# Kernel optimization log

Measured on AMD Instinct MI355X. Metric: run time of the kernel, lower is better.

The kernel has to match this reference:

```python
import jax, jax.numpy as jnp
import numpy as np

NUM_USERS = 100000
NUM_ITEMS = 50000
N_NODES = NUM_USERS + NUM_ITEMS
N_EDGES = 2400000
EMB = 64
BATCH = 4096
GCN_LAYERS = 3
TAU = 0.2
SSL_LAMBDA = 0.1
REG_LAMBDA = 1e-4


def setup_inputs() -> dict:
    key = jax.random.key(0)
    ks = jax.random.split(key, 8)
    user = jax.random.randint(ks[0], (BATCH,), 0, NUM_USERS, dtype=jnp.int32)
    pos_item = jax.random.randint(ks[1], (BATCH,), 0, NUM_ITEMS, dtype=jnp.int32)
    neg_item = jax.random.randint(ks[2], (BATCH,), 0, NUM_ITEMS, dtype=jnp.int32)
    # symmetric bipartite edges: user -> item and item -> user
    half = N_EDGES // 2
    src_u = jax.random.randint(ks[3], (half,), 0, NUM_USERS, dtype=jnp.int32)
    dst_i = jax.random.randint(ks[4], (half,), NUM_USERS, N_NODES, dtype=jnp.int32)
    adj_row = jnp.concatenate([src_u, dst_i])
    adj_col = jnp.concatenate([dst_i, src_u])
    # normalized-adjacency-like small positive values
    adj_val = jax.random.uniform(ks[5], (N_EDGES,), dtype=jnp.float32) * 0.01
    user_emb_w = jax.random.normal(ks[6], (NUM_USERS, EMB), dtype=jnp.float32) * 0.1
    item_emb_w = jax.random.normal(ks[7], (NUM_ITEMS, EMB), dtype=jnp.float32) * 0.1
    return {"user": user, "pos_item": pos_item, "neg_item": neg_item,
            "adj_row": adj_row, "adj_col": adj_col, "adj_val": adj_val,
            "user_emb_w": user_emb_w, "item_emb_w": item_emb_w}


def _aggregate(adj_row, adj_col, adj_val, user_emb_w, item_emb_w):
    emb = jnp.concatenate([user_emb_w, item_emb_w], axis=0)  # [N, d]
    acc = emb
    e = emb
    for _ in range(GCN_LAYERS):
        # sparse.mm(adj, e): gather columns, scale, scatter-add into rows
        e = jax.ops.segment_sum(adj_val[:, None] * e[adj_col], adj_row,
                                num_segments=N_NODES)
        acc = acc + e
    final = acc / (GCN_LAYERS + 1)  # mean over stacked layer outputs
    return final[:NUM_USERS], final[NUM_USERS:]


def reference(user, pos_item, neg_item, adj_row, adj_col, adj_val,
              user_emb_w, item_emb_w):
    user_all, item_all = _aggregate(adj_row, adj_col, adj_val,
                                    user_emb_w, item_emb_w)
    u = user_all[user]          # [B, d]
    pos = item_all[pos_item]    # [B, d]
    neg = item_all[neg_item]    # [B, d]
    # BPR loss
    pos_s = jnp.sum(u * pos, axis=-1)
    neg_s = jnp.sum(u * neg, axis=-1)
    bpr_loss = -jnp.mean(jax.nn.log_sigmoid(pos_s - neg_s))
    # L2 regularization
    b = u.shape[0]
    reg_loss = 0.5 * (jnp.sum(u * u) + jnp.sum(pos * pos) + jnp.sum(neg * neg)) / b
    reg_loss = reg_loss * REG_LAMBDA
    # neighbor-aggregate SSL (InfoNCE between user and its positive item)
    un = u / jnp.linalg.norm(u, axis=-1, keepdims=True)
    pn = pos / jnp.linalg.norm(pos, axis=-1, keepdims=True)
    logits = un @ pn.T / TAU                       # [B, B]
    pos_logit = jnp.diagonal(logits)
    na_loss = jnp.mean(jax.nn.logsumexp(logits, axis=1) - pos_logit) * SSL_LAMBDA
    return bpr_loss + reg_loss + na_loss
```

## Files before the change

### kernel.cpp

```cpp
#include <hip/hip_runtime.h>
#include <hip/hip_fp16.h>
#include <math.h>

#define NUM_USERS 100000
#define NUM_ITEMS 50000
#define N_NODES   150000
#define N_EDGES   2400000
#define HALF_E    (N_EDGES / 2)
#define EMB       64
#define BATCH     4096
#define TAU        0.2f
#define SSL_LAMBDA 0.1f
#define REG_LAMBDA 1e-4f

#define NB        293
#define BROWS     512
#define CAP       13632
#define BINA_BLK  512

__device__ __forceinline__ float wave_sum(float v) {
    #pragma unroll
    for (int m = 1; m < 64; m <<= 1) v += __shfl_xor(v, m, 64);
    return v;
}
__device__ __forceinline__ __half2 bits2h2(int b) {
    union { int i; __half2 h; } u; u.i = b; return u.h;
}
__device__ __forceinline__ int h22bits(__half2 h) {
    union { int i; __half2 h; } u; u.h = h; return u.i;
}
__device__ __forceinline__ float h2f(unsigned short s) {
    union { unsigned short s; __half h; } u; u.s = s; return __half2float(u.h);
}

__global__ __launch_bounds__(256) void cast_h0(
        const float4* __restrict__ uw, const float4* __restrict__ iw,
        uint2* __restrict__ h) {
    size_t i = (size_t)blockIdx.x * 256 + threadIdx.x;
    const size_t tot = (size_t)N_NODES * EMB / 4;
    if (i >= tot) return;
    const size_t nu = (size_t)NUM_USERS * EMB / 4;
    float4 v = (i < nu) ? uw[i] : iw[i - nu];
    h[i] = make_uint2(h22bits(__floats2half2_rn(v.x, v.y)),
                      h22bits(__floats2half2_rn(v.z, v.w)));
}

__global__ __launch_bounds__(256) void bin_scatter(
        const int* __restrict__ row, const int* __restrict__ col,
        const float* __restrict__ val,
        int* __restrict__ bucket_cursor, int2* __restrict__ arena) {
    __shared__ int hist[NB];
    const int t = threadIdx.x;
    for (int i = t; i < NB; i += 256) hist[i] = 0;
    __syncthreads();
    const int per = (HALF_E + gridDim.x - 1) / gridDim.x;
    const int beg = blockIdx.x * per;
    const int end = min(beg + per, HALF_E);
    for (int e = beg + t; e < end; e += 256) {
        int r = row[e], c = col[e];
        atomicAdd(&hist[r >> 9], 1);
        atomicAdd(&hist[c >> 9], 1);
    }
    __syncthreads();
    for (int i = t; i < NB; i += 256) {
        int cnt = hist[i];
        int base = cnt ? atomicAdd(&bucket_cursor[i], cnt) : 0;
        hist[i] = i * CAP + base;
    }
    __syncthreads();
    for (int e = beg + t; e < end; e += 256) {
        int r = row[e], c = col[e];
        float v1 = val[e], v2 = val[e + HALF_E];
        int s1 = atomicAdd(&hist[r >> 9], 1);
        int s2 = atomicAdd(&hist[c >> 9], 1);
        arena[s1] = make_int2(c | ((r & 511) << 18), __float_as_int(v1));
        arena[s2] = make_int2(r | ((c & 511) << 18), __float_as_int(v2));
    }
}

__global__ __launch_bounds__(256) void bucket_scan(
        const int* __restrict__ bucket_cursor, int* __restrict__ bucket_base,
        int* __restrict__ rowptr) {
    __shared__ int sm[256];
    const int t = threadIdx.x;
    const int K = (NB + 255) / 256;
    int v[K], s = 0;
    #pragma unroll
    for (int j = 0; j < K; j++) {
        int idx = t * K + j;
        v[j] = (idx < NB) ? bucket_cursor[idx] : 0;
        s += v[j];
    }
    sm[t] = s;
    __syncthreads();
    for (int m = 1; m < 256; m <<= 1) {
        int y = (t >= m) ? sm[t - m] : 0;
        __syncthreads();
        sm[t] += y;
        __syncthreads();
    }
    int excl = sm[t] - s;
    #pragma unroll
    for (int j = 0; j < K; j++) {
        int idx = t * K + j;
        if (idx < NB) bucket_base[idx] = excl;
        excl += v[j];
    }
    if (t == 0) rowptr[N_NODES] = N_EDGES;
}

__global__ __launch_bounds__(256) void bin_sort(
        const int* __restrict__ bucket_cursor, const int* __restrict__ bucket_base,
        const int2* __restrict__ arena,
        int* __restrict__ rowptr, int2* __restrict__ colval) {
    __shared__ int rcnt[BROWS];
    __shared__ int sm[256];
    const int bin = blockIdx.x;
    const int t = threadIdx.x;
    const int total = bucket_cursor[bin];
    const int count = min(total, CAP);
    const int gbase = bucket_base[bin];
    for (int i = t; i < BROWS; i += 256) rcnt[i] = 0;
    __syncthreads();
    for (int i = t; i < count; i += 256) {
        int rx = arena[bin * CAP + i].x >> 18;
        atomicAdd(&rcnt[rx], 1);
    }
    __syncthreads();
    int v0 = rcnt[2 * t], v1 = rcnt[2 * t + 1];
    int s = v0 + v1;
    sm[t] = s;
    __syncthreads();
    for (int m = 1; m < 256; m <<= 1) {
        int y = (t >= m) ? sm[t - m] : 0;
        __syncthreads();
        sm[t] += y;
        __syncthreads();
    }
    int excl = sm[t] - s;
    rcnt[2 * t] = excl;
    rcnt[2 * t + 1] = excl + v0;
    int r0 = bin * BROWS + 2 * t;
    if (r0 < N_NODES) rowptr[r0] = gbase + excl;
    if (r0 + 1 < N_NODES) rowptr[r0 + 1] = gbase + excl + v0;
    __syncthreads();
    for (int i = t; i < count; i += 256) {
        int2 rec = arena[bin * CAP + i];
        int pos = atomicAdd(&rcnt[rec.x >> 18], 1);
        __half2 hv = __float2half2_rn(__int_as_float(rec.y));
        colval[gbase + pos] = make_int2(rec.x & 0x3FFFF, h22bits(hv));
    }
    for (int i = count + t; i < total; i += 256)
        colval[gbase + i] = make_int2(0, 0);
}

__global__ __launch_bounds__(256) void spmm_csr(
        const int* __restrict__ rowptr, const int2* __restrict__ colval,
        const unsigned short* __restrict__ h_cur, unsigned short* __restrict__ h_next) {
    const int t = threadIdx.x;
    const int lane = t & 63;
    const int g = lane >> 4;
    const int l = lane & 15;
    int r = blockIdx.x * 4 + (t >> 6);
    if (r >= N_NODES) return;
    const int beg = rowptr[r], end = rowptr[r + 1];
    __half2 acc01 = __float2half2_rn(0.0f);
    __half2 acc23 = __float2half2_rn(0.0f);
    int e = beg + g;
    if (e < end) {
        int2 cv = colval[e];
        uint2 x = ((const uint2*)(h_cur + (size_t)cv.x * EMB))[l];
        e += 4;
        if (e < end) {
            int2 cv2 = colval[e];
            uint2 x2 = ((const uint2*)(h_cur + (size_t)cv2.x * EMB))[l];
            for (e += 4; e < end; e += 4) {
                int2 cv3 = colval[e];
                uint2 x3 = ((const uint2*)(h_cur + (size_t)cv3.x * EMB))[l];
                __half2 vv = bits2h2(cv.y);
                acc01 = __hfma2(vv, bits2h2(x.x), acc01);
                acc23 = __hfma2(vv, bits2h2(x.y), acc23);
                cv = cv2; x = x2; cv2 = cv3; x2 = x3;
            }
            __half2 vv = bits2h2(cv.y);
            acc01 = __hfma2(vv, bits2h2(x.x), acc01);
            acc23 = __hfma2(vv, bits2h2(x.y), acc23);
            cv = cv2; x = x2;
        }
        __half2 vv = bits2h2(cv.y);
        acc01 = __hfma2(vv, bits2h2(x.x), acc01);
        acc23 = __hfma2(vv, bits2h2(x.y), acc23);
    }
    int a0 = h22bits(acc01), a1 = h22bits(acc23);
    a0 = h22bits(__hadd2(bits2h2(a0), bits2h2(__shfl_xor(a0, 16, 64))));
    a1 = h22bits(__hadd2(bits2h2(a1), bits2h2(__shfl_xor(a1, 16, 64))));
    a0 = h22bits(__hadd2(bits2h2(a0), bits2h2(__shfl_xor(a0, 32, 64))));
    a1 = h22bits(__hadd2(bits2h2(a1), bits2h2(__shfl_xor(a1, 32, 64))));
    if (g == 0)
        ((uint2*)(h_next + (size_t)r * EMB))[l] = make_uint2(a0, a1);
}

__global__ __launch_bounds__(256) void spmm_sel(
        const int* __restrict__ rowptr, const int2* __restrict__ colval,
        const int* __restrict__ user, const int* __restrict__ pos,
        const int* __restrict__ neg,
        const unsigned short* __restrict__ h_cur, float* __restrict__ sel) {
    const int t = threadIdx.x;
    const int lane = t & 63;
    const int g = lane >> 4;
    const int l = lane & 15;
    int b = blockIdx.x * 4 + (t >> 6);
    if (b >= 3 * BATCH) return;
    int which = b / BATCH, bb = b - which * BATCH;
    int r = (which == 0) ? user[bb]
          : NUM_USERS + ((which == 1) ? pos[bb] : neg[bb]);
    const int beg = rowptr[r], end = rowptr[r + 1];
    __half2 acc01 = __float2half2_rn(0.0f);
    __half2 acc23 = __float2half2_rn(0.0f);
    int e = beg + g;
    if (e < end) {
        int2 cv = colval[e];
        uint2 x = ((const uint2*)(h_cur + (size_t)cv.x * EMB))[l];
        e += 4;
        if (e < end) {
            int2 cv2 = colval[e];
            uint2 x2 = ((const uint2*)(h_cur + (size_t)cv2.x * EMB))[l];
            for (e += 4; e < end; e += 4) {
                int2 cv3 = colval[e];
                uint2 x3 = ((const uint2*)(h_cur + (size_t)cv3.x * EMB))[l];
                __half2 vv = bits2h2(cv.y);
                acc01 = __hfma2(vv, bits2h2(x.x), acc01);
                acc23 = __hfma2(vv, bits2h2(x.y), acc23);
                cv = cv2; x = x2; cv2 = cv3; x2 = x3;
            }
            __half2 vv = bits2h2(cv.y);
            acc01 = __hfma2(vv, bits2h2(x.x), acc01);
            acc23 = __hfma2(vv, bits2h2(x.y), acc23);
            cv = cv2; x = x2;
        }
        __half2 vv = bits2h2(cv.y);
        acc01 = __hfma2(vv, bits2h2(x.x), acc01);
        acc23 = __hfma2(vv, bits2h2(x.y), acc23);
    }
    int a0 = h22bits(acc01), a1 = h22bits(acc23);
    a0 = h22bits(__hadd2(bits2h2(a0), bits2h2(__shfl_xor(a0, 16, 64))));
    a1 = h22bits(__hadd2(bits2h2(a1), bits2h2(__shfl_xor(a1, 16, 64))));
    a0 = h22bits(__hadd2(bits2h2(a0), bits2h2(__shfl_xor(a0, 32, 64))));
    a1 = h22bits(__hadd2(bits2h2(a1), bits2h2(__shfl_xor(a1, 32, 64))));
    if (g == 0) {
        float2 f01 = __half22float2(bits2h2(a0));
        float2 f23 = __half22float2(bits2h2(a1));
        uint2 hx = ((const uint2*)(h_cur + (size_t)r * EMB))[l];
        float2 s01 = __half22float2(bits2h2((int)hx.x));
        float2 s23 = __half22float2(bits2h2((int)hx.y));
        float4* dst = (float4*)(sel + (size_t)b * EMB);
        float4 old = dst[l];
        old.x += f01.x + s01.x; old.y += f01.y + s01.y;
        old.z += f23.x + s23.x; old.w += f23.y + s23.y;
        dst[l] = old;
    }
}

__global__ __launch_bounds__(256) void gather_add_w(
        const int* __restrict__ user, const int* __restrict__ pos,
        const int* __restrict__ neg,
        const float* __restrict__ uw, const float* __restrict__ iw,
        float* __restrict__ sel) {
    const int lane = threadIdx.x & 63;
    int wid = blockIdx.x * (blockDim.x >> 6) + (threadIdx.x >> 6);
    if (wid >= 3 * BATCH) return;
    int which = wid / BATCH, b = wid - which * BATCH;
    const float* src;
    if (which == 0) { int n = user[b]; src = uw + (size_t)n * EMB; }
    else { int n = (which == 1) ? pos[b] : neg[b]; src = iw + (size_t)n * EMB; }
    sel[(size_t)wid * EMB + lane] = src[lane];
}

__global__ __launch_bounds__(256) void gather_add_h(
        const int* __restrict__ user, const int* __restrict__ pos,
        const int* __restrict__ neg,
        const unsigned short* __restrict__ h, float* __restrict__ sel) {
    const int lane = threadIdx.x & 63;
    int wid = blockIdx.x * (blockDim.x >> 6) + (threadIdx.x >> 6);
    if (wid >= 3 * BATCH) return;
    int which = wid / BATCH, b = wid - which * BATCH;
    int node = (which == 0) ? user[b]
             : NUM_USERS + ((which == 1) ? pos[b] : neg[b]);
    sel[(size_t)wid * EMB + lane] += h2f(h[(size_t)node * EMB + lane]);
}

__global__ __launch_bounds__(256) void batch_loss(
        const float* __restrict__ sel,
        float* __restrict__ un, float* __restrict__ pn,
        float* __restrict__ diag,
        float* __restrict__ pbpr, float* __restrict__ preg) {
    __shared__ float lb[4], lr[4];
    const int t = threadIdx.x;
    const int lane = t & 63;
    const int w = t >> 6;
    int b = blockIdx.x * 4 + w;
    const float inv4 = 0.25f;
    float u = sel[(size_t)b * EMB + lane] * inv4;
    float p = sel[(size_t)(BATCH + b) * EMB + lane] * inv4;
    float n = sel[(size_t)(2 * BATCH + b) * EMB + lane] * inv4;
    float pos_s = wave_sum(u * p);
    float neg_s = wave_sum(u * n);
    float uu = wave_sum(u * u);
    float pp = wave_sum(p * p);
    float nn = wave_sum(n * n);
    float ru = rsqrtf(uu), rp = rsqrtf(pp);
    un[(size_t)b * EMB + lane] = u * ru;
    pn[(size_t)b * EMB + lane] = p * rp;
    if (lane == 0) {
        diag[b] = pos_s * ru * rp * (1.0f / TAU);
        float d = pos_s - neg_s;
        float tt = -d;
        lb[w] = fmaxf(tt, 0.0f) + log1pf(expf(-fabsf(tt)));
        lr[w] = uu + pp + nn;
    }
    __syncthreads();
    if (t == 0) {
        pbpr[blockIdx.x] = lb[0] + lb[1] + lb[2] + lb[3];
        preg[blockIdx.x] = lr[0] + lr[1] + lr[2] + lr[3];
    }
}

#define TS 128
__global__ __launch_bounds__(256) void ssl_gemm(
        const float* __restrict__ un, const float* __restrict__ pn,
        float* __restrict__ rowsum_p) {
    __shared__ float ua[EMB][TS];
    __shared__ float pb[EMB][TS];
    const int t = threadIdx.x;
    const int it = blockIdx.x & 31, jt = blockIdx.x >> 5;
    const int i0 = it * TS;
    const int j0 = jt * TS;
    for (int x = t; x < TS * 16; x += 256) {
        int i = x & (TS - 1), d4 = x >> 7;
        float4 v = ((const float4*)(un + (size_t)(i0 + i) * EMB))[d4];
        ua[d4 * 4 + 0][i] = v.x; ua[d4 * 4 + 1][i] = v.y;
        ua[d4 * 4 + 2][i] = v.z; ua[d4 * 4 + 3][i] = v.w;
        float4 w = ((const float4*)(pn + (size_t)(j0 + i) * EMB))[d4];
        pb[d4 * 4 + 0][i] = w.x; pb[d4 * 4 + 1][i] = w.y;
        pb[d4 * 4 + 2][i] = w.z; pb[d4 * 4 + 3][i] = w.w;
    }
    __syncthreads();
    const int tx = t & 15, ty = t >> 4;
    float c[8][8];
    #pragma unroll
    for (int p = 0; p < 8; p++)
        #pragma unroll
        for (int q = 0; q < 8; q++) c[p][q] = 0.0f;
    for (int k = 0; k < EMB; k++) {
        float a[8], b[8];
        #pragma unroll
        for (int q = 0; q < 8; q++) { a[q] = ua[k][ty * 8 + q]; b[q] = pb[k][tx * 8 + q]; }
        #pragma unroll
        for (int p = 0; p < 8; p++)
            #pragma unroll
            for (int q = 0; q < 8; q++) c[p][q] = fmaf(a[p], b[q], c[p][q]);
    }
    float s[8];
    #pragma unroll
    for (int p = 0; p < 8; p++) {
        s[p] = 0.0f;
        #pragma unroll
        for (int q = 0; q < 8; q++) s[p] += expf(c[p][q] * (1.0f / TAU));
    }
    #pragma unroll
    for (int m = 1; m < 16; m <<= 1)
        #pragma unroll
        for (int p = 0; p < 8; p++) s[p] += __shfl_xor(s[p], m, 64);
    if (tx == 0) {
        #pragma unroll
        for (int p = 0; p < 8; p++)
            rowsum_p[(size_t)jt * BATCH + i0 + ty * 8 + p] = s[p];
    }
}

__global__ __launch_bounds__(256) void finalize(
        const float* __restrict__ rowsum_p, const float* __restrict__ diag,
        const float* __restrict__ pbpr, const float* __restrict__ preg,
        float* __restrict__ out) {
    __shared__ float red[3][4];
    const int t = threadIdx.x;
    float sb = 0.0f, sr = 0.0f, ss = 0.0f;
    for (int i = t; i < BATCH / 4; i += 256) { sb += pbpr[i]; sr += preg[i]; }
    for (int i = t; i < BATCH; i += 256) {
        float rs = 0.0f;
        #pragma unroll
        for (int j = 0; j < 32; j++) rs += rowsum_p[(size_t)j * BATCH + i];
        ss += logf(rs) - diag[i];
    }
    sb = wave_sum(sb); sr = wave_sum(sr); ss = wave_sum(ss);
    const int w = t >> 6;
    if ((t & 63) == 0) { red[0][w] = sb; red[1][w] = sr; red[2][w] = ss; }
    __syncthreads();
    if (t == 0) {
        float bpr_sum = red[0][0] + red[0][1] + red[0][2] + red[0][3];
        float reg_sum = red[1][0] + red[1][1] + red[1][2] + red[1][3];
        float ssl_sum = red[2][0] + red[2][1] + red[2][2] + red[2][3];
        float bpr = bpr_sum * (1.0f / BATCH);
        float reg = 0.5f * reg_sum * (1.0f / BATCH) * REG_LAMBDA;
        float ssl = ssl_sum * (1.0f / BATCH) * SSL_LAMBDA;
        out[0] = bpr + reg + ssl;
    }
}

extern "C" void kernel_launch(void* const* d_in, const int* in_sizes, int n_in,
                              void* d_out, int out_size, void* d_ws, size_t ws_size,
                              hipStream_t stream) {
    const int*   user    = (const int*)d_in[0];
    const int*   pos     = (const int*)d_in[1];
    const int*   neg     = (const int*)d_in[2];
    const int*   adj_row = (const int*)d_in[3];
    const int*   adj_col = (const int*)d_in[4];
    const float* adj_val = (const float*)d_in[5];
    const float* user_w  = (const float*)d_in[6];
    const float* item_w  = (const float*)d_in[7];
    float* out = (float*)d_out;

    unsigned short* hA = (unsigned short*)d_ws;
    unsigned short* hB = hA + (size_t)N_NODES * EMB;
    float* buf1   = (float*)d_ws + (size_t)N_NODES * EMB;
    float* sel    = buf1 + (size_t)N_NODES * EMB;
    float* un     = sel  + (size_t)3 * BATCH * EMB;
    float* pn     = un   + (size_t)BATCH * EMB;
    float* diag   = pn   + (size_t)BATCH * EMB;
    float* rowsum_p = diag + BATCH;
    float* pbpr   = rowsum_p + 32 * BATCH;
    float* preg   = pbpr + 1024;
    int*   rowptr = (int*)(preg + 1024);
    int*   bucket_cursor = rowptr + 150016;
    int*   bucket_base   = bucket_cursor + 512;
    int2*  colval = (int2*)(bucket_base + 512);
    int2*  arena  = (int2*)buf1;

    hipMemsetAsync(bucket_cursor, 0, 512 * sizeof(int), stream);

    dim3 blk(256);

    const int cast_blocks = (int)(((size_t)N_NODES * EMB / 4 + 255) / 256);
    cast_h0<<<cast_blocks, blk, 0, stream>>>((const float4*)user_w,
                                             (const float4*)item_w, (uint2*)hA);

    bin_scatter<<<BINA_BLK, blk, 0, stream>>>(adj_row, adj_col, adj_val,
                                              bucket_cursor, arena);
    bucket_scan<<<1, blk, 0, stream>>>(bucket_cursor, bucket_base, rowptr);
    bin_sort<<<NB, blk, 0, stream>>>(bucket_cursor, bucket_base, arena,
                                     rowptr, colval);

    const int gw_blocks = (3 * BATCH) / 4;
    gather_add_w<<<gw_blocks, blk, 0, stream>>>(user, pos, neg, user_w, item_w, sel);

    spmm_csr<<<(N_NODES + 3) / 4, blk, 0, stream>>>(rowptr, colval, hA, hB);
    gather_add_h<<<gw_blocks, blk, 0, stream>>>(user, pos, neg, hB, sel);
    spmm_csr<<<(N_NODES + 3) / 4, blk, 0, stream>>>(rowptr, colval, hB, hA);
    spmm_sel<<<(3 * BATCH + 3) / 4, blk, 0, stream>>>(rowptr, colval, user, pos,
                                                      neg, hA, sel);

    batch_loss<<<BATCH / 4, blk, 0, stream>>>(sel, un, pn, diag, pbpr, preg);
    ssl_gemm<<<(BATCH / TS) * (BATCH / TS), blk, 0, stream>>>(un, pn, rowsum_p);
    finalize<<<1, blk, 0, stream>>>(rowsum_p, diag, pbpr, preg, out);
}
```

Measured before the change: 378.7 us.

## Fuse cast with bin scatter, widen SpMM loads, fold gathers into loss

The fp16 cast kernel and the edge bin scatter now run in one launch, with the first 512 blocks also doing the binning. The SpMM kernels use 8 lanes per edge with 16-byte loads and 8 edges in flight per wave instead of 4. The separate gather kernels for layer 0 and layer 1 are removed: batch_loss reads the original weights and the layer-1 half buffer directly, and spmm_sel writes its result instead of doing a read-modify-write. The SSL exp switches to the fast __expf, and the fused prep kernel gives the binning blocks extra work before they start.

```diff
diff --git a/kernel.cpp b/kernel.cpp
--- a/kernel.cpp
+++ b/kernel.cpp
@@ -17,6 +17,7 @@
 #define BROWS     512
 #define CAP       13632
 #define BINA_BLK  512
+#define CAST_BLK  9375
 
 __device__ __forceinline__ float wave_sum(float v) {
     #pragma unroll
@@ -33,27 +34,26 @@
     union { unsigned short s; __half h; } u; u.s = s; return __half2float(u.h);
 }
 
-__global__ __launch_bounds__(256) void cast_h0(
-        const float4* __restrict__ uw, const float4* __restrict__ iw,
-        uint2* __restrict__ h) {
-    size_t i = (size_t)blockIdx.x * 256 + threadIdx.x;
-    const size_t tot = (size_t)N_NODES * EMB / 4;
-    if (i >= tot) return;
-    const size_t nu = (size_t)NUM_USERS * EMB / 4;
-    float4 v = (i < nu) ? uw[i] : iw[i - nu];
-    h[i] = make_uint2(h22bits(__floats2half2_rn(v.x, v.y)),
-                      h22bits(__floats2half2_rn(v.z, v.w)));
-}
-
-__global__ __launch_bounds__(256) void bin_scatter(
+__global__ __launch_bounds__(256) void prep_kernel(
+        const float4* __restrict__ uw4, const float4* __restrict__ iw4,
+        uint2* __restrict__ h,
         const int* __restrict__ row, const int* __restrict__ col,
         const float* __restrict__ val,
         int* __restrict__ bucket_cursor, int2* __restrict__ arena) {
     __shared__ int hist[NB];
     const int t = threadIdx.x;
-    for (int i = t; i < NB; i += 256) hist[i] = 0;
-    __syncthreads();
-    const int per = (HALF_E + gridDim.x - 1) / gridDim.x;
+    size_t i = (size_t)blockIdx.x * 256 + t;
+    const size_t tot = (size_t)N_NODES * EMB / 4;
+    if (i < tot) {
+        const size_t nu = (size_t)NUM_USERS * EMB / 4;
+        float4 v = (i < nu) ? uw4[i] : iw4[i - nu];
+        h[i] = make_uint2(h22bits(__floats2half2_rn(v.x, v.y)),
+                          h22bits(__floats2half2_rn(v.z, v.w)));
+    }
+    if (blockIdx.x >= BINA_BLK) return;
+    for (int k = t; k < NB; k += 256) hist[k] = 0;
+    __syncthreads();
+    const int per = (HALF_E + BINA_BLK - 1) / BINA_BLK;
     const int beg = blockIdx.x * per;
     const int end = min(beg + per, HALF_E);
     for (int e = beg + t; e < end; e += 256) {
@@ -62,10 +62,10 @@
         atomicAdd(&hist[c >> 9], 1);
     }
     __syncthreads();
-    for (int i = t; i < NB; i += 256) {
-        int cnt = hist[i];
-        int base = cnt ? atomicAdd(&bucket_cursor[i], cnt) : 0;
-        hist[i] = i * CAP + base;
+    for (int k = t; k < NB; k += 256) {
+        int cnt = hist[k];
+        int base = cnt ? atomicAdd(&bucket_cursor[k], cnt) : 0;
+        hist[k] = k * CAP + base;
     }
     __syncthreads();
     for (int e = beg + t; e < end; e += 256) {
@@ -159,45 +159,54 @@
         const unsigned short* __restrict__ h_cur, unsigned short* __restrict__ h_next) {
     const int t = threadIdx.x;
     const int lane = t & 63;
-    const int g = lane >> 4;
-    const int l = lane & 15;
+    const int g = lane >> 3;
+    const int l = lane & 7;
     int r = blockIdx.x * 4 + (t >> 6);
     if (r >= N_NODES) return;
     const int beg = rowptr[r], end = rowptr[r + 1];
-    __half2 acc01 = __float2half2_rn(0.0f);
-    __half2 acc23 = __float2half2_rn(0.0f);
+    __half2 ac0 = __float2half2_rn(0.0f), ac1 = ac0, ac2 = ac0, ac3 = ac0;
     int e = beg + g;
     if (e < end) {
         int2 cv = colval[e];
-        uint2 x = ((const uint2*)(h_cur + (size_t)cv.x * EMB))[l];
-        e += 4;
+        uint4 x = ((const uint4*)(h_cur + (size_t)cv.x * EMB))[l];
+        e += 8;
         if (e < end) {
             int2 cv2 = colval[e];
-            uint2 x2 = ((const uint2*)(h_cur + (size_t)cv2.x * EMB))[l];
-            for (e += 4; e < end; e += 4) {
+            uint4 x2 = ((const uint4*)(h_cur + (size_t)cv2.x * EMB))[l];
+            for (e += 8; e < end; e += 8) {
                 int2 cv3 = colval[e];
-                uint2 x3 = ((const uint2*)(h_cur + (size_t)cv3.x * EMB))[l];
+                uint4 x3 = ((const uint4*)(h_cur + (size_t)cv3.x * EMB))[l];
                 __half2 vv = bits2h2(cv.y);
-                acc01 = __hfma2(vv, bits2h2(x.x), acc01);
-                acc23 = __hfma2(vv, bits2h2(x.y), acc23);
+                ac0 = __hfma2(vv, bits2h2(x.x), ac0);
+                ac1 = __hfma2(vv, bits2h2(x.y), ac1);
+                ac2 = __hfma2(vv, bits2h2(x.z), ac2);
+                ac3 = __hfma2(vv, bits2h2(x.w), ac3);
                 cv = cv2; x = x2; cv2 = cv3; x2 = x3;
             }
             __half2 vv = bits2h2(cv.y);
-            acc01 = __hfma2(vv, bits2h2(x.x), acc01);
-            acc23 = __hfma2(vv, bits2h2(x.y), acc23);
+            ac0 = __hfma2(vv, bits2h2(x.x), ac0);
+            ac1 = __hfma2(vv, bits2h2(x.y), ac1);
+            ac2 = __hfma2(vv, bits2h2(x.z), ac2);
+            ac3 = __hfma2(vv, bits2h2(x.w), ac3);
             cv = cv2; x = x2;
         }
         __half2 vv = bits2h2(cv.y);
-        acc01 = __hfma2(vv, bits2h2(x.x), acc01);
-        acc23 = __hfma2(vv, bits2h2(x.y), acc23);
-    }
-    int a0 = h22bits(acc01), a1 = h22bits(acc23);
-    a0 = h22bits(__hadd2(bits2h2(a0), bits2h2(__shfl_xor(a0, 16, 64))));
-    a1 = h22bits(__hadd2(bits2h2(a1), bits2h2(__shfl_xor(a1, 16, 64))));
-    a0 = h22bits(__hadd2(bits2h2(a0), bits2h2(__shfl_xor(a0, 32, 64))));
-    a1 = h22bits(__hadd2(bits2h2(a1), bits2h2(__shfl_xor(a1, 32, 64))));
+        ac0 = __hfma2(vv, bits2h2(x.x), ac0);
+        ac1 = __hfma2(vv, bits2h2(x.y), ac1);
+        ac2 = __hfma2(vv, bits2h2(x.z), ac2);
+        ac3 = __hfma2(vv, bits2h2(x.w), ac3);
+    }
+    int a0 = h22bits(ac0), a1 = h22bits(ac1), a2 = h22bits(ac2), a3 = h22bits(ac3);
+    #pragma unroll
+    for (int m = 8; m < 64; m <<= 1) {
+        a0 = h22bits(__hadd2(bits2h2(a0), bits2h2(__shfl_xor(a0, m, 64))));
+        a1 = h22bits(__hadd2(bits2h2(a1), bits2h2(__shfl_xor(a1, m, 64))));
+        a2 = h22bits(__hadd2(bits2h2(a2), bits2h2(__shfl_xor(a2, m, 64))));
+        a3 = h22bits(__hadd2(bits2h2(a3), bits2h2(__shfl_xor(a3, m, 64))));
+    }
     if (g == 0)
-        ((uint2*)(h_next + (size_t)r * EMB))[l] = make_uint2(a0, a1);
+        ((uint4*)(h_next + (size_t)r * EMB))[l] =
+            make_uint4((unsigned)a0, (unsigned)a1, (unsigned)a2, (unsigned)a3);
 }
 
 __global__ __launch_bounds__(256) void spmm_sel(
@@ -207,89 +216,75 @@
         const unsigned short* __restrict__ h_cur, float* __restrict__ sel) {
     const int t = threadIdx.x;
     const int lane = t & 63;
-    const int g = lane >> 4;
-    const int l = lane & 15;
+    const int g = lane >> 3;
+    const int l = lane & 7;
     int b = blockIdx.x * 4 + (t >> 6);
     if (b >= 3 * BATCH) return;
     int which = b / BATCH, bb = b - which * BATCH;
     int r = (which == 0) ? user[bb]
           : NUM_USERS + ((which == 1) ? pos[bb] : neg[bb]);
     const int beg = rowptr[r], end = rowptr[r + 1];
-    __half2 acc01 = __float2half2_rn(0.0f);
-    __half2 acc23 = __float2half2_rn(0.0f);
+    __half2 ac0 = __float2half2_rn(0.0f), ac1 = ac0, ac2 = ac0, ac3 = ac0;
     int e = beg + g;
     if (e < end) {
         int2 cv = colval[e];
-        uint2 x = ((const uint2*)(h_cur + (size_t)cv.x * EMB))[l];
-        e += 4;
+        uint4 x = ((const uint4*)(h_cur + (size_t)cv.x * EMB))[l];
+        e += 8;
         if (e < end) {
             int2 cv2 = colval[e];
-            uint2 x2 = ((const uint2*)(h_cur + (size_t)cv2.x * EMB))[l];
-            for (e += 4; e < end; e += 4) {
+            uint4 x2 = ((const uint4*)(h_cur + (size_t)cv2.x * EMB))[l];
+            for (e += 8; e < end; e += 8) {
                 int2 cv3 = colval[e];
-                uint2 x3 = ((const uint2*)(h_cur + (size_t)cv3.x * EMB))[l];
+                uint4 x3 = ((const uint4*)(h_cur + (size_t)cv3.x * EMB))[l];
                 __half2 vv = bits2h2(cv.y);
-                acc01 = __hfma2(vv, bits2h2(x.x), acc01);
-                acc23 = __hfma2(vv, bits2h2(x.y), acc23);
+                ac0 = __hfma2(vv, bits2h2(x.x), ac0);
+                ac1 = __hfma2(vv, bits2h2(x.y), ac1);
+                ac2 = __hfma2(vv, bits2h2(x.z), ac2);
+                ac3 = __hfma2(vv, bits2h2(x.w), ac3);
                 cv = cv2; x = x2; cv2 = cv3; x2 = x3;
             }
             __half2 vv = bits2h2(cv.y);
-            acc01 = __hfma2(vv, bits2h2(x.x), acc01);
-            acc23 = __hfma2(vv, bits2h2(x.y), acc23);
+            ac0 = __hfma2(vv, bits2h2(x.x), ac0);
+            ac1 = __hfma2(vv, bits2h2(x.y), ac1);
+            ac2 = __hfma2(vv, bits2h2(x.z), ac2);
+            ac3 = __hfma2(vv, bits2h2(x.w), ac3);
             cv = cv2; x = x2;
         }
         __half2 vv = bits2h2(cv.y);
-        acc01 = __hfma2(vv, bits2h2(x.x), acc01);
-        acc23 = __hfma2(vv, bits2h2(x.y), acc23);
-    }
-    int a0 = h22bits(acc01), a1 = h22bits(acc23);
-    a0 = h22bits(__hadd2(bits2h2(a0), bits2h2(__shfl_xor(a0, 16, 64))));
-    a1 = h22bits(__hadd2(bits2h2(a1), bits2h2(__shfl_xor(a1, 16, 64))));
-    a0 = h22bits(__hadd2(bits2h2(a0), bits2h2(__shfl_xor(a0, 32, 64))));
-    a1 = h22bits(__hadd2(bits2h2(a1), bits2h2(__shfl_xor(a1, 32, 64))));
+        ac0 = __hfma2(vv, bits2h2(x.x), ac0);
+        ac1 = __hfma2(vv, bits2h2(x.y), ac1);
+        ac2 = __hfma2(vv, bits2h2(x.z), ac2);
+        ac3 = __hfma2(vv, bits2h2(x.w), ac3);
+    }
+    int a0 = h22bits(ac0), a1 = h22bits(ac1), a2 = h22bits(ac2), a3 = h22bits(ac3);
+    #pragma unroll
+    for (int m = 8; m < 64; m <<= 1) {
+        a0 = h22bits(__hadd2(bits2h2(a0), bits2h2(__shfl_xor(a0, m, 64))));
+        a1 = h22bits(__hadd2(bits2h2(a1), bits2h2(__shfl_xor(a1, m, 64))));
+        a2 = h22bits(__hadd2(bits2h2(a2), bits2h2(__shfl_xor(a2, m, 64))));
+        a3 = h22bits(__hadd2(bits2h2(a3), bits2h2(__shfl_xor(a3, m, 64))));
+    }
     if (g == 0) {
-        float2 f01 = __half22float2(bits2h2(a0));
-        float2 f23 = __half22float2(bits2h2(a1));
-        uint2 hx = ((const uint2*)(h_cur + (size_t)r * EMB))[l];
-        float2 s01 = __half22float2(bits2h2((int)hx.x));
-        float2 s23 = __half22float2(bits2h2((int)hx.y));
+        float2 f0 = __half22float2(bits2h2(a0));
+        float2 f1 = __half22float2(bits2h2(a1));
+        float2 f2 = __half22float2(bits2h2(a2));
+        float2 f3 = __half22float2(bits2h2(a3));
+        uint4 hx = ((const uint4*)(h_cur + (size_t)r * EMB))[l];
+        float2 s0 = __half22float2(bits2h2((int)hx.x));
+        float2 s1 = __half22float2(bits2h2((int)hx.y));
+        float2 s2 = __half22float2(bits2h2((int)hx.z));
+        float2 s3 = __half22float2(bits2h2((int)hx.w));
         float4* dst = (float4*)(sel + (size_t)b * EMB);
-        float4 old = dst[l];
-        old.x += f01.x + s01.x; old.y += f01.y + s01.y;
-        old.z += f23.x + s23.x; old.w += f23.y + s23.y;
-        dst[l] = old;
-    }
-}
-
-__global__ __launch_bounds__(256) void gather_add_w(
+        dst[2 * l]     = make_float4(f0.x + s0.x, f0.y + s0.y, f1.x + s1.x, f1.y + s1.y);
+        dst[2 * l + 1] = make_float4(f2.x + s2.x, f2.y + s2.y, f3.x + s3.x, f3.y + s3.y);
+    }
+}
+
+__global__ __launch_bounds__(256) void batch_loss(
         const int* __restrict__ user, const int* __restrict__ pos,
         const int* __restrict__ neg,
         const float* __restrict__ uw, const float* __restrict__ iw,
-        float* __restrict__ sel) {
-    const int lane = threadIdx.x & 63;
-    int wid = blockIdx.x * (blockDim.x >> 6) + (threadIdx.x >> 6);
-    if (wid >= 3 * BATCH) return;
-    int which = wid / BATCH, b = wid - which * BATCH;
-    const float* src;
-    if (which == 0) { int n = user[b]; src = uw + (size_t)n * EMB; }
-    else { int n = (which == 1) ? pos[b] : neg[b]; src = iw + (size_t)n * EMB; }
-    sel[(size_t)wid * EMB + lane] = src[lane];
-}
-
-__global__ __launch_bounds__(256) void gather_add_h(
-        const int* __restrict__ user, const int* __restrict__ pos,
-        const int* __restrict__ neg,
-        const unsigned short* __restrict__ h, float* __restrict__ sel) {
-    const int lane = threadIdx.x & 63;
-    int wid = blockIdx.x * (blockDim.x >> 6) + (threadIdx.x >> 6);
-    if (wid >= 3 * BATCH) return;
-    int which = wid / BATCH, b = wid - which * BATCH;
-    int node = (which == 0) ? user[b]
-             : NUM_USERS + ((which == 1) ? pos[b] : neg[b]);
-    sel[(size_t)wid * EMB + lane] += h2f(h[(size_t)node * EMB + lane]);
-}
-
-__global__ __launch_bounds__(256) void batch_loss(
+        const unsigned short* __restrict__ h1,
         const float* __restrict__ sel,
         float* __restrict__ un, float* __restrict__ pn,
         float* __restrict__ diag,
@@ -300,9 +295,16 @@
     const int w = t >> 6;
     int b = blockIdx.x * 4 + w;
     const float inv4 = 0.25f;
-    float u = sel[(size_t)b * EMB + lane] * inv4;
-    float p = sel[(size_t)(BATCH + b) * EMB + lane] * inv4;
-    float n = sel[(size_t)(2 * BATCH + b) * EMB + lane] * inv4;
+    int nu = user[b], np = pos[b], ng = neg[b];
+    float u = (uw[(size_t)nu * EMB + lane]
+             + h2f(h1[(size_t)nu * EMB + lane])
+             + sel[(size_t)b * EMB + lane]) * inv4;
+    float p = (iw[(size_t)np * EMB + lane]
+             + h2f(h1[(size_t)(NUM_USERS + np) * EMB + lane])
+             + sel[(size_t)(BATCH + b) * EMB + lane]) * inv4;
+    float n = (iw[(size_t)ng * EMB + lane]
+             + h2f(h1[(size_t)(NUM_USERS + ng) * EMB + lane])
+             + sel[(size_t)(2 * BATCH + b) * EMB + lane]) * inv4;
     float pos_s = wave_sum(u * p);
     float neg_s = wave_sum(u * n);
     float uu = wave_sum(u * u);
@@ -365,7 +367,7 @@
     for (int p = 0; p < 8; p++) {
         s[p] = 0.0f;
         #pragma unroll
-        for (int q = 0; q < 8; q++) s[p] += expf(c[p][q] * (1.0f / TAU));
+        for (int q = 0; q < 8; q++) s[p] += __expf(c[p][q] * (1.0f / TAU));
     }
     #pragma unroll
     for (int m = 1; m < 16; m <<= 1)
@@ -440,26 +442,21 @@
 
     dim3 blk(256);
 
-    const int cast_blocks = (int)(((size_t)N_NODES * EMB / 4 + 255) / 256);
-    cast_h0<<<cast_blocks, blk, 0, stream>>>((const float4*)user_w,
-                                             (const float4*)item_w, (uint2*)hA);
-
-    bin_scatter<<<BINA_BLK, blk, 0, stream>>>(adj_row, adj_col, adj_val,
+    prep_kernel<<<CAST_BLK, blk, 0, stream>>>((const float4*)user_w,
+                                              (const float4*)item_w, (uint2*)hA,
+                                              adj_row, adj_col, adj_val,
                                               bucket_cursor, arena);
     bucket_scan<<<1, blk, 0, stream>>>(bucket_cursor, bucket_base, rowptr);
     bin_sort<<<NB, blk, 0, stream>>>(bucket_cursor, bucket_base, arena,
                                      rowptr, colval);
 
-    const int gw_blocks = (3 * BATCH) / 4;
-    gather_add_w<<<gw_blocks, blk, 0, stream>>>(user, pos, neg, user_w, item_w, sel);
-
     spmm_csr<<<(N_NODES + 3) / 4, blk, 0, stream>>>(rowptr, colval, hA, hB);
-    gather_add_h<<<gw_blocks, blk, 0, stream>>>(user, pos, neg, hB, sel);
     spmm_csr<<<(N_NODES + 3) / 4, blk, 0, stream>>>(rowptr, colval, hB, hA);
     spmm_sel<<<(3 * BATCH + 3) / 4, blk, 0, stream>>>(rowptr, colval, user, pos,
                                                       neg, hA, sel);
 
-    batch_loss<<<BATCH / 4, blk, 0, stream>>>(sel, un, pn, diag, pbpr, preg);
+    batch_loss<<<BATCH / 4, blk, 0, stream>>>(user, pos, neg, user_w, item_w,
+                                              hB, sel, un, pn, diag, pbpr, preg);
     ssl_gemm<<<(BATCH / TS) * (BATCH / TS), blk, 0, stream>>>(un, pn, rowsum_p);
     finalize<<<1, blk, 0, stream>>>(rowsum_p, diag, pbpr, preg, out);
 }
```

New measurement: 333.8 us. 11.9% less time.
